# Kernel tuning notes

Hardware: AMD Instinct MI355X
Metric: run time of the kernel (lower is better)

The kernel has to match this reference:

```python
import jax, jax.numpy as jnp
import numpy as np

NUM_PARTS = 8
JOINTS_TO_PARTS = {0: [0, 1, 2, 3, 4], 1: [5, 6, 11, 12], 2: [5, 7, 9], 3: [6, 8, 10],
                   4: [11, 13, 15], 5: [12, 14, 16], 6: [15, 17, 18, 19], 7: [16, 20, 21, 22]}

# (8, 23) one-hot aggregation matrix: part_heatmap = sum of member joint heatmaps
_AGG = np.zeros((NUM_PARTS, 23), dtype=np.float32)
for _p, _js in JOINTS_TO_PARTS.items():
    _AGG[_p, _js] = 1.0
AGG = jnp.asarray(_AGG)


def setup_inputs() -> dict:
    key = jax.random.key(0)
    k1, k2 = jax.random.split(key)
    pred_masks = jax.random.uniform(k1, (32, 9, 256, 256), dtype=jnp.float32)
    pred_keypoints = jax.random.uniform(k2, (32, 23, 256, 256), dtype=jnp.float32)
    return {"pred_masks": pred_masks, "pred_keypoints": pred_keypoints}


def _centers(x, thresh):
    # x: (b, p, h, w) -> (b, p, 2) centroid of pixels above thresh.
    # Matches torch.nonzero semantics: coord 0 is the h index, coord 1 the w index;
    # empty mask -> nan mean -> (nan > 0) False -> center stays 0; mean==0 also stays 0.
    b, p, h, w = x.shape
    m = (x > thresh).astype(x.dtype)                      # (b,p,h,w)
    cnt = m.sum(axis=(-2, -1))                            # (b,p)
    rows = jnp.arange(h, dtype=x.dtype)
    cols = jnp.arange(w, dtype=x.dtype)
    sx = jnp.einsum('bphw,h->bp', m, rows)                # sum of h-indices
    sy = jnp.einsum('bphw,w->bp', m, cols)                # sum of w-indices
    safe = jnp.maximum(cnt, 1.0)
    mx, my = sx / safe, sy / safe
    valid = cnt > 0
    cx = jnp.where(valid & (mx > 0), mx, 0.0)
    cy = jnp.where(valid & (my > 0), my, 0.0)
    return jnp.stack([cx, cy], axis=-1)                   # (b,p,2)


def reference(pred_masks, pred_keypoints):
    # Part mask centers: channels 1..8 (channel 0 is background)
    mask_centers = _centers(pred_masks[:, 1:1 + NUM_PARTS], 0.5)          # (b,8,2)
    # Keypoint part heatmaps: sum member joint heatmaps per part
    part_hm = jnp.einsum('pk,bkhw->bphw', AGG, pred_keypoints)            # (b,8,h,w)
    kp_centers = _centers(part_hm, 0.3)                                   # (b,8,2)
    # code: invalid if any coord is exactly 0 in either center
    code = jnp.any((kp_centers == 0) | (mask_centers == 0), axis=2)       # (b,8)
    loss = (mask_centers - kp_centers) ** 2                               # (b,8,2) MSE 'none'
    valid = (~code).astype(loss.dtype)                                    # (b,8)
    num = (loss * valid[..., None]).sum()
    den = valid.sum() * 2.0                                               # 2 coords per valid entry
    return 1e-05 * (num / den)
```

## Files before the change

kernel.cpp:

```cpp
#include <hip/hip_runtime.h>

#define HW 65536
#define GROUPS (HW / 4)
#define NMASK_CH 9
#define NKP_CH 23
#define NPARTS 8
#define NB 32

__device__ __forceinline__ void f4add(float4& a, const float4 b) {
    a.x += b.x; a.y += b.y; a.z += b.z; a.w += b.w;
}

__global__ __launch_bounds__(256) void mask_stats_kernel(
    const float* __restrict__ masks, int* __restrict__ stats) {
    const int b = blockIdx.z, p = blockIdx.y, chunk = blockIdx.x;
    const float4* plane =
        (const float4*)(masks + ((size_t)b * NMASK_CH + (1 + p)) * HW);
    int cnt = 0, sx = 0, sy = 0;
    const int g0 = chunk * 4096 + threadIdx.x;
#pragma unroll
    for (int j = 0; j < 16; ++j) {
        const int g = g0 + j * 256;
        const float4 v = plane[g];
        const int base = g * 4;
        const int h = base >> 8, w0 = base & 255;
        if (v.x > 0.5f) { cnt++; sx += h; sy += w0; }
        if (v.y > 0.5f) { cnt++; sx += h; sy += w0 + 1; }
        if (v.z > 0.5f) { cnt++; sx += h; sy += w0 + 2; }
        if (v.w > 0.5f) { cnt++; sx += h; sy += w0 + 3; }
    }
#pragma unroll
    for (int off = 32; off; off >>= 1) {
        cnt += __shfl_down(cnt, off);
        sx  += __shfl_down(sx, off);
        sy  += __shfl_down(sy, off);
    }
    __shared__ int sh[3];
    if (threadIdx.x < 3) sh[threadIdx.x] = 0;
    __syncthreads();
    if ((threadIdx.x & 63) == 0) {
        atomicAdd(&sh[0], cnt);
        atomicAdd(&sh[1], sx);
        atomicAdd(&sh[2], sy);
    }
    __syncthreads();
    if (threadIdx.x < 3)
        atomicAdd(&stats[(b * NPARTS + p) * 3 + threadIdx.x], sh[threadIdx.x]);
}

__global__ __launch_bounds__(256) void kp_stats_kernel(
    const float* __restrict__ kp, int* __restrict__ stats) {
    const int b = blockIdx.y, chunk = blockIdx.x;
    const float4* kb = (const float4*)(kp + (size_t)b * NKP_CH * HW);

    int cnt[NPARTS], sx[NPARTS], sy[NPARTS];
#pragma unroll
    for (int p = 0; p < NPARTS; ++p) { cnt[p] = 0; sx[p] = 0; sy[p] = 0; }

#pragma unroll
    for (int j = 0; j < 2; ++j) {
        const int g = chunk * 512 + j * 256 + threadIdx.x;
        float4 s0, s1, s2, s3, s4, s5, s6, s7, v;
#define LD(K) kb[(K) * GROUPS + g]
        s0 = LD(0);
        v = LD(1); f4add(s0, v);
        v = LD(2); f4add(s0, v);
        v = LD(3); f4add(s0, v);
        v = LD(4); f4add(s0, v);
        v = LD(5); s1 = v; s2 = v;
        v = LD(6); f4add(s1, v); s3 = v;
        v = LD(7); f4add(s2, v);
        v = LD(8); f4add(s3, v);
        v = LD(9); f4add(s2, v);
        v = LD(10); f4add(s3, v);
        v = LD(11); f4add(s1, v); s4 = v;
        v = LD(12); f4add(s1, v); s5 = v;
        v = LD(13); f4add(s4, v);
        v = LD(14); f4add(s5, v);
        v = LD(15); f4add(s4, v); s6 = v;
        v = LD(16); f4add(s5, v); s7 = v;
        v = LD(17); f4add(s6, v);
        v = LD(18); f4add(s6, v);
        v = LD(19); f4add(s6, v);
        v = LD(20); f4add(s7, v);
        v = LD(21); f4add(s7, v);
        v = LD(22); f4add(s7, v);
#undef LD
        const int base = g * 4;
        const int h = base >> 8, w0 = base & 255;
#define TALLY(P, S)                                           \
        if ((S).x > 0.3f) { cnt[P]++; sx[P] += h; sy[P] += w0; }     \
        if ((S).y > 0.3f) { cnt[P]++; sx[P] += h; sy[P] += w0 + 1; } \
        if ((S).z > 0.3f) { cnt[P]++; sx[P] += h; sy[P] += w0 + 2; } \
        if ((S).w > 0.3f) { cnt[P]++; sx[P] += h; sy[P] += w0 + 3; }
        TALLY(0, s0) TALLY(1, s1) TALLY(2, s2) TALLY(3, s3)
        TALLY(4, s4) TALLY(5, s5) TALLY(6, s6) TALLY(7, s7)
#undef TALLY
    }

#pragma unroll
    for (int p = 0; p < NPARTS; ++p) {
#pragma unroll
        for (int off = 32; off; off >>= 1) {
            cnt[p] += __shfl_down(cnt[p], off);
            sx[p]  += __shfl_down(sx[p], off);
            sy[p]  += __shfl_down(sy[p], off);
        }
    }
    __shared__ int sh[NPARTS * 3];
    if (threadIdx.x < NPARTS * 3) sh[threadIdx.x] = 0;
    __syncthreads();
    if ((threadIdx.x & 63) == 0) {
#pragma unroll
        for (int p = 0; p < NPARTS; ++p) {
            atomicAdd(&sh[p * 3 + 0], cnt[p]);
            atomicAdd(&sh[p * 3 + 1], sx[p]);
            atomicAdd(&sh[p * 3 + 2], sy[p]);
        }
    }
    __syncthreads();
    if (threadIdx.x < NPARTS * 3) {
        atomicAdd(&stats[768 + b * NPARTS * 3 + threadIdx.x], sh[threadIdx.x]);
    }
}

__global__ __launch_bounds__(256) void finish_kernel(
    const int* __restrict__ stats, float* __restrict__ out) {
    const int t = threadIdx.x;
    const int cm  = stats[t * 3 + 0];
    const int sxm = stats[t * 3 + 1];
    const int sym = stats[t * 3 + 2];
    const int ck  = stats[768 + t * 3 + 0];
    const int sxk = stats[768 + t * 3 + 1];
    const int syk = stats[768 + t * 3 + 2];

    const float cxm = (cm > 0 && sxm > 0) ? (float)sxm / (float)cm : 0.0f;
    const float cym = (cm > 0 && sym > 0) ? (float)sym / (float)cm : 0.0f;
    const float cxk = (ck > 0 && sxk > 0) ? (float)sxk / (float)ck : 0.0f;
    const float cyk = (ck > 0 && syk > 0) ? (float)syk / (float)ck : 0.0f;

    const bool code = (cxm == 0.0f) || (cym == 0.0f) ||
                      (cxk == 0.0f) || (cyk == 0.0f);
    double num = 0.0, nv = 0.0;
    if (!code) {
        const double dx = (double)cxm - (double)cxk;
        const double dy = (double)cym - (double)cyk;
        num = dx * dx + dy * dy;
        nv = 1.0;
    }
#pragma unroll
    for (int off = 32; off; off >>= 1) {
        num += __shfl_down(num, off);
        nv  += __shfl_down(nv, off);
    }
    __shared__ double sh[8];
    const int wave = t >> 6;
    if ((t & 63) == 0) { sh[wave * 2] = num; sh[wave * 2 + 1] = nv; }
    __syncthreads();
    if (t == 0) {
        const double N = sh[0] + sh[2] + sh[4] + sh[6];
        const double V = sh[1] + sh[3] + sh[5] + sh[7];
        out[0] = (float)(1e-5 * (N / (V * 2.0)));
    }
}

extern "C" void kernel_launch(void* const* d_in, const int* in_sizes, int n_in,
                              void* d_out, int out_size, void* d_ws, size_t ws_size,
                              hipStream_t stream) {
    const float* masks = (const float*)d_in[0];
    const float* kp    = (const float*)d_in[1];
    float* out = (float*)d_out;
    int* stats = (int*)d_ws;

    hipMemsetAsync(d_ws, 0, 1536 * sizeof(int), stream);
    hipLaunchKernelGGL(mask_stats_kernel, dim3(4, NPARTS, NB), dim3(256), 0,
                       stream, masks, stats);
    hipLaunchKernelGGL(kp_stats_kernel, dim3(32, NB), dim3(256), 0,
                       stream, kp, stats);
    hipLaunchKernelGGL(finish_kernel, dim3(1), dim3(256), 0, stream, stats, out);
}
```

Measured before the change: 318.0 us.

## Fuse mask and keypoint stats kernels, drop memset and atomics, use nontemporal loads

Merges the mask and keypoint statistic kernels into one launch of 1280 blocks. Each block writes its partial sums to its own slot, so the workspace memset and the global atomics go away, and the finish kernel adds up the 32 keypoint chunk partials itself. Input reads now use nontemporal vector loads. Each mask block now covers a whole plane, which gives fewer, longer blocks and may leave the work less evenly spread across CUs.

Result: faster. 286.2 us (-10.0%).

```diff
diff --git a/kernel.cpp b/kernel.cpp
--- a/kernel.cpp
+++ b/kernel.cpp
@@ -1,138 +1,147 @@
 #include <hip/hip_runtime.h>
 
 #define HW 65536
-#define GROUPS (HW / 4)
+#define GROUPS 16384
 #define NMASK_CH 9
 #define NKP_CH 23
 #define NPARTS 8
 #define NB 32
 
-__device__ __forceinline__ void f4add(float4& a, const float4 b) {
-    a.x += b.x; a.y += b.y; a.z += b.z; a.w += b.w;
+#define KP_OFF 768
+
+typedef float vf4 __attribute__((ext_vector_type(4)));
+
+__device__ __forceinline__ vf4 ntload(const float* p) {
+    return __builtin_nontemporal_load((const vf4*)p);
 }
 
-__global__ __launch_bounds__(256) void mask_stats_kernel(
-    const float* __restrict__ masks, int* __restrict__ stats) {
-    const int b = blockIdx.z, p = blockIdx.y, chunk = blockIdx.x;
-    const float4* plane =
-        (const float4*)(masks + ((size_t)b * NMASK_CH + (1 + p)) * HW);
-    int cnt = 0, sx = 0, sy = 0;
-    const int g0 = chunk * 4096 + threadIdx.x;
+__global__ __launch_bounds__(256) void stats_kernel(
+    const float* __restrict__ masks, const float* __restrict__ kp,
+    int* __restrict__ stats) {
+    const int tid = threadIdx.x;
+    const int bid = blockIdx.x;
+    const int wave = tid >> 6;
+    __shared__ int sh[4][NPARTS * 3];
+
+    if (bid < 256) {
+        const int b = bid >> 3, p = bid & 7;
+        const float* plane = masks + ((size_t)b * NMASK_CH + 1 + p) * HW;
+        int cnt = 0, sx = 0, sy = 0;
+#pragma unroll 8
+        for (int j = 0; j < 64; ++j) {
+            const int g = tid + j * 256;
+            const vf4 v = ntload(plane + (size_t)g * 4);
+            const int base = g * 4;
+            const int h = base >> 8, w0 = base & 255;
+            if (v.x > 0.5f) { cnt++; sx += h; sy += w0; }
+            if (v.y > 0.5f) { cnt++; sx += h; sy += w0 + 1; }
+            if (v.z > 0.5f) { cnt++; sx += h; sy += w0 + 2; }
+            if (v.w > 0.5f) { cnt++; sx += h; sy += w0 + 3; }
+        }
 #pragma unroll
-    for (int j = 0; j < 16; ++j) {
-        const int g = g0 + j * 256;
-        const float4 v = plane[g];
-        const int base = g * 4;
-        const int h = base >> 8, w0 = base & 255;
-        if (v.x > 0.5f) { cnt++; sx += h; sy += w0; }
-        if (v.y > 0.5f) { cnt++; sx += h; sy += w0 + 1; }
-        if (v.z > 0.5f) { cnt++; sx += h; sy += w0 + 2; }
-        if (v.w > 0.5f) { cnt++; sx += h; sy += w0 + 3; }
-    }
+        for (int off = 32; off; off >>= 1) {
+            cnt += __shfl_down(cnt, off);
+            sx  += __shfl_down(sx, off);
+            sy  += __shfl_down(sy, off);
+        }
+        if ((tid & 63) == 0) {
+            sh[wave][0] = cnt; sh[wave][1] = sx; sh[wave][2] = sy;
+        }
+        __syncthreads();
+        if (tid < 3)
+            stats[bid * 3 + tid] =
+                sh[0][tid] + sh[1][tid] + sh[2][tid] + sh[3][tid];
+    } else {
+        const int id = bid - 256;
+        const int b = id >> 5, c = id & 31;
+        const float* kb = kp + (size_t)b * NKP_CH * HW;
+
+        int cnt[NPARTS], sx[NPARTS], sy[NPARTS];
 #pragma unroll
-    for (int off = 32; off; off >>= 1) {
-        cnt += __shfl_down(cnt, off);
-        sx  += __shfl_down(sx, off);
-        sy  += __shfl_down(sy, off);
-    }
-    __shared__ int sh[3];
-    if (threadIdx.x < 3) sh[threadIdx.x] = 0;
-    __syncthreads();
-    if ((threadIdx.x & 63) == 0) {
-        atomicAdd(&sh[0], cnt);
-        atomicAdd(&sh[1], sx);
-        atomicAdd(&sh[2], sy);
-    }
-    __syncthreads();
-    if (threadIdx.x < 3)
-        atomicAdd(&stats[(b * NPARTS + p) * 3 + threadIdx.x], sh[threadIdx.x]);
-}
-
-__global__ __launch_bounds__(256) void kp_stats_kernel(
-    const float* __restrict__ kp, int* __restrict__ stats) {
-    const int b = blockIdx.y, chunk = blockIdx.x;
-    const float4* kb = (const float4*)(kp + (size_t)b * NKP_CH * HW);
-
-    int cnt[NPARTS], sx[NPARTS], sy[NPARTS];
-#pragma unroll
-    for (int p = 0; p < NPARTS; ++p) { cnt[p] = 0; sx[p] = 0; sy[p] = 0; }
+        for (int p = 0; p < NPARTS; ++p) { cnt[p] = 0; sx[p] = 0; sy[p] = 0; }
 
 #pragma unroll
-    for (int j = 0; j < 2; ++j) {
-        const int g = chunk * 512 + j * 256 + threadIdx.x;
-        float4 s0, s1, s2, s3, s4, s5, s6, s7, v;
-#define LD(K) kb[(K) * GROUPS + g]
-        s0 = LD(0);
-        v = LD(1); f4add(s0, v);
-        v = LD(2); f4add(s0, v);
-        v = LD(3); f4add(s0, v);
-        v = LD(4); f4add(s0, v);
-        v = LD(5); s1 = v; s2 = v;
-        v = LD(6); f4add(s1, v); s3 = v;
-        v = LD(7); f4add(s2, v);
-        v = LD(8); f4add(s3, v);
-        v = LD(9); f4add(s2, v);
-        v = LD(10); f4add(s3, v);
-        v = LD(11); f4add(s1, v); s4 = v;
-        v = LD(12); f4add(s1, v); s5 = v;
-        v = LD(13); f4add(s4, v);
-        v = LD(14); f4add(s5, v);
-        v = LD(15); f4add(s4, v); s6 = v;
-        v = LD(16); f4add(s5, v); s7 = v;
-        v = LD(17); f4add(s6, v);
-        v = LD(18); f4add(s6, v);
-        v = LD(19); f4add(s6, v);
-        v = LD(20); f4add(s7, v);
-        v = LD(21); f4add(s7, v);
-        v = LD(22); f4add(s7, v);
+        for (int j = 0; j < 2; ++j) {
+            const int g = c * 512 + j * 256 + tid;
+            vf4 s0, s1, s2, s3, s4, s5, s6, s7, v;
+#define LD(K) ntload(kb + (size_t)((K) * GROUPS + g) * 4)
+            s0 = LD(0);
+            v = LD(1); s0 += v;
+            v = LD(2); s0 += v;
+            v = LD(3); s0 += v;
+            v = LD(4); s0 += v;
+            v = LD(5); s1 = v; s2 = v;
+            v = LD(6); s1 += v; s3 = v;
+            v = LD(7); s2 += v;
+            v = LD(8); s3 += v;
+            v = LD(9); s2 += v;
+            v = LD(10); s3 += v;
+            v = LD(11); s1 += v; s4 = v;
+            v = LD(12); s1 += v; s5 = v;
+            v = LD(13); s4 += v;
+            v = LD(14); s5 += v;
+            v = LD(15); s4 += v; s6 = v;
+            v = LD(16); s5 += v; s7 = v;
+            v = LD(17); s6 += v;
+            v = LD(18); s6 += v;
+            v = LD(19); s6 += v;
+            v = LD(20); s7 += v;
+            v = LD(21); s7 += v;
+            v = LD(22); s7 += v;
 #undef LD
-        const int base = g * 4;
-        const int h = base >> 8, w0 = base & 255;
-#define TALLY(P, S)                                           \
-        if ((S).x > 0.3f) { cnt[P]++; sx[P] += h; sy[P] += w0; }     \
-        if ((S).y > 0.3f) { cnt[P]++; sx[P] += h; sy[P] += w0 + 1; } \
-        if ((S).z > 0.3f) { cnt[P]++; sx[P] += h; sy[P] += w0 + 2; } \
-        if ((S).w > 0.3f) { cnt[P]++; sx[P] += h; sy[P] += w0 + 3; }
-        TALLY(0, s0) TALLY(1, s1) TALLY(2, s2) TALLY(3, s3)
-        TALLY(4, s4) TALLY(5, s5) TALLY(6, s6) TALLY(7, s7)
+            const int base = g * 4;
+            const int h = base >> 8, w0 = base & 255;
+#define TALLY(P, S)                                                  \
+            if ((S).x > 0.3f) { cnt[P]++; sx[P] += h; sy[P] += w0; }     \
+            if ((S).y > 0.3f) { cnt[P]++; sx[P] += h; sy[P] += w0 + 1; } \
+            if ((S).z > 0.3f) { cnt[P]++; sx[P] += h; sy[P] += w0 + 2; } \
+            if ((S).w > 0.3f) { cnt[P]++; sx[P] += h; sy[P] += w0 + 3; }
+            TALLY(0, s0) TALLY(1, s1) TALLY(2, s2) TALLY(3, s3)
+            TALLY(4, s4) TALLY(5, s5) TALLY(6, s6) TALLY(7, s7)
 #undef TALLY
-    }
+        }
 
 #pragma unroll
-    for (int p = 0; p < NPARTS; ++p) {
+        for (int p = 0; p < NPARTS; ++p) {
 #pragma unroll
-        for (int off = 32; off; off >>= 1) {
-            cnt[p] += __shfl_down(cnt[p], off);
-            sx[p]  += __shfl_down(sx[p], off);
-            sy[p]  += __shfl_down(sy[p], off);
+            for (int off = 32; off; off >>= 1) {
+                cnt[p] += __shfl_down(cnt[p], off);
+                sx[p]  += __shfl_down(sx[p], off);
+                sy[p]  += __shfl_down(sy[p], off);
+            }
         }
-    }
-    __shared__ int sh[NPARTS * 3];
-    if (threadIdx.x < NPARTS * 3) sh[threadIdx.x] = 0;
-    __syncthreads();
-    if ((threadIdx.x & 63) == 0) {
+        if ((tid & 63) == 0) {
 #pragma unroll
-        for (int p = 0; p < NPARTS; ++p) {
-            atomicAdd(&sh[p * 3 + 0], cnt[p]);
-            atomicAdd(&sh[p * 3 + 1], sx[p]);
-            atomicAdd(&sh[p * 3 + 2], sy[p]);
+            for (int p = 0; p < NPARTS; ++p) {
+                sh[wave][p * 3 + 0] = cnt[p];
+                sh[wave][p * 3 + 1] = sx[p];
+                sh[wave][p * 3 + 2] = sy[p];
+            }
         }
-    }
-    __syncthreads();
-    if (threadIdx.x < NPARTS * 3) {
-        atomicAdd(&stats[768 + b * NPARTS * 3 + threadIdx.x], sh[threadIdx.x]);
+        __syncthreads();
+        if (tid < NPARTS * 3)
+            stats[KP_OFF + id * 24 + tid] =
+                sh[0][tid] + sh[1][tid] + sh[2][tid] + sh[3][tid];
     }
 }
 
 __global__ __launch_bounds__(256) void finish_kernel(
     const int* __restrict__ stats, float* __restrict__ out) {
     const int t = threadIdx.x;
+    const int b = t >> 3, p = t & 7;
+
     const int cm  = stats[t * 3 + 0];
     const int sxm = stats[t * 3 + 1];
     const int sym = stats[t * 3 + 2];
-    const int ck  = stats[768 + t * 3 + 0];
-    const int sxk = stats[768 + t * 3 + 1];
-    const int syk = stats[768 + t * 3 + 2];
+
+    int ck = 0, sxk = 0, syk = 0;
+#pragma unroll
+    for (int c = 0; c < 32; ++c) {
+        const int base = KP_OFF + (b * 32 + c) * 24 + p * 3;
+        ck  += stats[base + 0];
+        sxk += stats[base + 1];
+        syk += stats[base + 2];
+    }
 
     const float cxm = (cm > 0 && sxm > 0) ? (float)sxm / (float)cm : 0.0f;
     const float cym = (cm > 0 && sym > 0) ? (float)sym / (float)cm : 0.0f;
@@ -172,10 +181,7 @@
     float* out = (float*)d_out;
     int* stats = (int*)d_ws;
 
-    hipMemsetAsync(d_ws, 0, 1536 * sizeof(int), stream);
-    hipLaunchKernelGGL(mask_stats_kernel, dim3(4, NPARTS, NB), dim3(256), 0,
-                       stream, masks, stats);
-    hipLaunchKernelGGL(kp_stats_kernel, dim3(32, NB), dim3(256), 0,
-                       stream, kp, stats);
+    hipLaunchKernelGGL(stats_kernel, dim3(1280), dim3(256), 0, stream,
+                       masks, kp, stats);
     hipLaunchKernelGGL(finish_kernel, dim3(1), dim3(256), 0, stream, stats, out);
 }
```
